# Kernel tuning notes

Hardware: AMD Instinct MI355X
Metric: run time of the kernel (lower is better)

Reference implementation:

```python
import jax, jax.numpy as jnp
import numpy as np

DT = 0.1
BOX = 1.0  # WORLD_SIZE
EPS = 1e-6


def range_angle(ang):
    return jnp.mod(ang + jnp.pi, 2.0 * jnp.pi) - jnp.pi


def ekf_step(x, P, a, Y, n1, n2_sigma, n2_kappa, gains, obs_gains):
    # x: (N,5) [px,py,ang,vel,ang_vel]; P: (N,5,5); a: (N,2); Y: (2,N)
    N = x.shape[0]
    dt = DT
    og = obs_gains

    # --- noise-free dynamics (w=0 in original forward) ---
    vel = gains[0] * a[:, 0]
    ang_vel = gains[1] * a[:, 1]
    ang = range_angle(x[:, 2] + ang_vel * dt)
    px = jnp.clip(x[:, 0] + vel * jnp.cos(ang) * dt, -BOX, BOX)
    py = jnp.clip(x[:, 1] + vel * jnp.sin(ang) * dt, -BOX, BOX)
    x_ = jnp.stack([px, py, ang, vel, ang_vel], axis=1)  # (N,5)

    # --- Jacobian A (N,5,5): eye(3) block + two trig entries ---
    d3 = jnp.arange(3)
    A = jnp.zeros((N, 5, 5), x.dtype)
    A = A.at[:, d3, d3].set(1.0)
    A = A.at[:, 0, 2].set(-vel * jnp.sin(ang) * dt)
    A = A.at[:, 1, 2].set(vel * jnp.cos(ang) * dt)

    # --- predict: L is identity in the original code, so L Q L^T = Q ---
    Q = jnp.diag(jnp.exp(2.0 * n1))
    P_ = jnp.einsum('nij,njk,nlk->nil', A, P, A) + Q  # (N,5,5)

    # --- innovation covariance S = H P_ H^T + M R M^T (R = I, M diag) ---
    # H = [0 | diag(og)] so H P_ H^T = diag(og) P_[3:5,3:5] diag(og)
    HPHt = P_[:, 3:5, 3:5] * og[None, :, None] * og[None, None, :]
    m_diag = x_[:, 3:5] ** 2 * jnp.exp(2.0 * n2_kappa) + jnp.exp(2.0 * n2_sigma)
    S = HPHt + m_diag[:, :, None] * jnp.eye(2, dtype=x.dtype)  # (N,2,2)

    # --- explicit 2x2 inverse ---
    sa, sb = S[:, 0, 0], S[:, 0, 1]
    sc, sd = S[:, 1, 0], S[:, 1, 1]
    det = sa * sd - sb * sc
    Sinv = jnp.stack([jnp.stack([sd, -sb], -1), jnp.stack([-sc, sa], -1)], -2)
    Sinv = Sinv / det[:, None, None]

    # --- Kalman gain K = P_ H^T S^{-1} ---
    PHt = P_[:, :, 3:5] * og[None, None, :]  # (N,5,2)
    K = jnp.einsum('nij,njk->nik', PHt, Sinv)  # (N,5,2)

    # --- update ---
    h = og[None, :] * x_[:, 3:5]  # noise-free observations (N,2)
    err = Y.T - h
    x_new = x_ + jnp.einsum('nij,nj->ni', K, err)

    KH = jnp.zeros((N, 5, 5), x.dtype).at[:, :, 3:5].set(K * og[None, None, :])
    I_KH = jnp.eye(5, dtype=x.dtype) - KH
    P_new = jnp.einsum('nij,njk->nik', I_KH, P_)
    P_new = 0.5 * (P_new + jnp.swapaxes(P_new, -1, -2)) + EPS * jnp.eye(5, dtype=x.dtype)
    return x_new, P_new, K


def setup_inputs() -> dict:
    key = jax.random.key(0)
    ks = jax.random.split(key, 6)
    N = 500_000
    x = jax.random.normal(ks[0], (N, 5), jnp.float32)
    # symmetric positive-definite covariances
    Lr = 0.1 * jax.random.normal(ks[1], (N, 5, 5), jnp.float32)
    P = jnp.einsum('nij,nkj->nik', Lr, Lr) + 0.5 * jnp.eye(5, dtype=jnp.float32)
    a = jax.random.normal(ks[2], (N, 2), jnp.float32)
    Y = 0.5 * jax.random.normal(ks[3], (2, N), jnp.float32)
    n1 = jnp.full((5,), -1.0, jnp.float32)
    n2 = jnp.full((4,), -1.0, jnp.float32)
    return {
        'x': x, 'P': P, 'a': a, 'Y': Y,
        'n1': n1,
        'n2_sigma': n2[:2],
        'n2_kappa': n2[2:],
        'gains': jnp.ones((2,), jnp.float32),
        'obs_gains': jnp.ones((2,), jnp.float32),
    }


def reference(x, P, a, Y, n1, n2_sigma, n2_kappa, gains, obs_gains):
    return ekf_step(x, P, a, Y, n1, n2_sigma, n2_kappa, gains, obs_gains)
```

## Files before the change

kernel.cpp:

```cpp
#include <hip/hip_runtime.h>
#include <math.h>
#include <stdint.h>


#define BLK 64
#define SLICE_F 2560

__global__ __launch_bounds__(256) void ekf_kernel(
    const float* __restrict__ xg, const float* __restrict__ Pg,
    const float* __restrict__ ag, const float* __restrict__ Yg,
    const float* __restrict__ n1, const float* __restrict__ n2s,
    const float* __restrict__ n2k, const float* __restrict__ gains,
    const float* __restrict__ og, float* __restrict__ out, int N)
{
    __shared__ float4 ldsv[4 * (SLICE_F / 4)];
    const int tid = threadIdx.x;
    const int wv = tid >> 6, l = tid & 63;
    float* s = (float*)ldsv + wv * SLICE_F;

    const int tiles = (N + BLK - 1) / BLK;
    const int tile = blockIdx.x * 4 + wv;
    if (tile >= tiles) return;
    const int base = tile * BLK;

    const float dt = 0.1f;
    const float fPI  = 3.14159265358979323846f;
    const float f2PI = 6.28318530717958647692f;
    const float EPS_ = 1e-6f;

    const float g0 = gains[0], g1 = gains[1];
    const float og0 = og[0], og1 = og[1];
    const float q0 = expf(2.f * n1[0]), q1 = expf(2.f * n1[1]),
                q2 = expf(2.f * n1[2]), q3 = expf(2.f * n1[3]),
                q4 = expf(2.f * n1[4]);
    const float e2s0 = expf(2.f * n2s[0]), e2s1 = expf(2.f * n2s[1]);
    const float e2k0 = expf(2.f * n2k[0]), e2k1 = expf(2.f * n2k[1]);

    if (base + BLK <= N) {
        const float4* p4 = (const float4*)(Pg + (size_t)base * 25);
        float4 v0 = p4[0 * 64 + l];
        float4 v1 = p4[1 * 64 + l];
        float4 v2 = p4[2 * 64 + l];
        float4 v3 = p4[3 * 64 + l];
        float4 v4 = p4[4 * 64 + l];
        float4 v5 = p4[5 * 64 + l];
        float  vr = (Pg + (size_t)base * 25)[1536 + l];
        float4 xv = ((const float4*)(xg + (size_t)base * 5))[l];
        float  xr = (xg + (size_t)base * 5)[256 + l];
        float2 av = ((const float2*)(ag + (size_t)base * 2))[l];
        float  y0 = Yg[base + l];
        float  y1 = Yg[N + base + l];

        float4* s4 = (float4*)s;
        s4[0 * 64 + l] = v0; s4[1 * 64 + l] = v1; s4[2 * 64 + l] = v2;
        s4[3 * 64 + l] = v3; s4[4 * 64 + l] = v4; s4[5 * 64 + l] = v5;
        s[1536 + l] = vr;
        ((float4*)(s + 1600))[l] = xv;
        s[1856 + l] = xr;

        const float* pr = s + l * 25;
        float p00 = pr[0],  p01 = pr[1],  p02 = pr[2];
        float p10 = pr[5],  p11 = pr[6],  p12 = pr[7];
        float p20 = pr[10], p21 = pr[11], p22 = pr[12];
        const float* xp = s + 1600 + l * 5;
        float x0 = xp[0], x1 = xp[1], x2 = xp[2];

        float vel = g0 * av.x, angvel = g1 * av.y;

        float ar = x2 + angvel * dt + fPI;
        float w = fmodf(ar, f2PI);
        if (w < 0.0f) w += f2PI;
        float ang = w - fPI;

        float sn, cs;
        sincosf(ang, &sn, &cs);

        float px = fminf(fmaxf(x0 + vel * cs * dt, -1.0f), 1.0f);
        float py = fminf(fmaxf(x1 + vel * sn * dt, -1.0f), 1.0f);

        float m0 = -vel * sn * dt, m1 = vel * cs * dt;

        float b00 = p00 + m0 * p20, b01 = p01 + m0 * p21, b02 = p02 + m0 * p22;
        float b10 = p10 + m1 * p20, b11 = p11 + m1 * p21, b12 = p12 + m1 * p22;
        float t00 = b00 + m0 * b02, t01 = b01 + m1 * b02;
        float t10 = b10 + m0 * b12, t11 = b11 + m1 * b12;
        float t20 = p20 + m0 * p22, t21 = p21 + m1 * p22, t22 = p22;
        float t02 = b02, t12 = b12;

        t00 += q0; t11 += q1; t22 += q2;
        float s01 = 0.5f * (t01 + t10);
        float s02 = 0.5f * (t02 + t20);
        float s12 = 0.5f * (t12 + t21);
        t00 += EPS_; t11 += EPS_; t22 += EPS_;

        float S00 = q3 * og0 * og0 + vel * vel * e2k0 + e2s0;
        float S11 = q4 * og1 * og1 + angvel * angvel * e2k1 + e2s1;
        float K30 = q3 * og0 / S00;
        float K41 = q4 * og1 / S11;

        float xn3 = vel    + K30 * (y0 - og0 * vel);
        float xn4 = angvel + K41 * (y1 - og1 * angvel);
        float Pn33 = (1.0f - K30 * og0) * q3 + EPS_;
        float Pn44 = (1.0f - K41 * og1) * q4 + EPS_;

        float* xx = s + l * 5;
        xx[0] = px; xx[1] = py; xx[2] = ang; xx[3] = xn3; xx[4] = xn4;
        float* pp = s + 320 + l * 25;
        pp[0]  = t00; pp[1]  = s01; pp[2]  = s02; pp[3]  = 0.f; pp[4]  = 0.f;
        pp[5]  = s01; pp[6]  = t11; pp[7]  = s12; pp[8]  = 0.f; pp[9]  = 0.f;
        pp[10] = s02; pp[11] = s12; pp[12] = t22; pp[13] = 0.f; pp[14] = 0.f;
        pp[15] = 0.f; pp[16] = 0.f; pp[17] = 0.f; pp[18] = Pn33; pp[19] = 0.f;
        pp[20] = 0.f; pp[21] = 0.f; pp[22] = 0.f; pp[23] = 0.f; pp[24] = Pn44;
        float* kk = s + 1920 + l * 10;
        kk[0] = 0.f; kk[1] = 0.f; kk[2] = 0.f; kk[3] = 0.f; kk[4] = 0.f;
        kk[5] = 0.f; kk[6] = K30; kk[7] = 0.f; kk[8] = 0.f; kk[9] = K41;

        float4* gx4 = (float4*)(out + (size_t)base * 5);
        float4* gp4 = (float4*)(out + (size_t)5 * N + (size_t)base * 25);
        float4* gk4 = (float4*)(out + (size_t)30 * N + (size_t)base * 10);
        const float4* lx4 = (const float4*)s;
        const float4* lp4 = (const float4*)(s + 320);
        const float4* lk4 = (const float4*)(s + 1920);
        gx4[l] = lx4[l];
        if (l < 16) gx4[64 + l] = lx4[64 + l];
        #pragma unroll
        for (int j = 0; j < 6; ++j) gp4[j * 64 + l] = lp4[j * 64 + l];
        if (l < 16) gp4[384 + l] = lp4[384 + l];
        #pragma unroll
        for (int j = 0; j < 2; ++j) gk4[j * 64 + l] = lk4[j * 64 + l];
        if (l < 32) gk4[128 + l] = lk4[128 + l];
    } else {
        const int i = base + l;
        if (i < N) {
            const float* pr = Pg + (size_t)i * 25;
            float p00 = pr[0],  p01 = pr[1],  p02 = pr[2];
            float p10 = pr[5],  p11 = pr[6],  p12 = pr[7];
            float p20 = pr[10], p21 = pr[11], p22 = pr[12];
            float x0 = xg[i * 5 + 0], x1 = xg[i * 5 + 1], x2 = xg[i * 5 + 2];
            float a0 = ag[i * 2 + 0], a1 = ag[i * 2 + 1];
            float y0 = Yg[i], y1 = Yg[N + i];

            float vel = g0 * a0, angvel = g1 * a1;
            float ar = x2 + angvel * dt + fPI;
            float w = fmodf(ar, f2PI);
            if (w < 0.0f) w += f2PI;
            float ang = w - fPI;
            float sn, cs;
            sincosf(ang, &sn, &cs);
            float px = fminf(fmaxf(x0 + vel * cs * dt, -1.0f), 1.0f);
            float py = fminf(fmaxf(x1 + vel * sn * dt, -1.0f), 1.0f);
            float m0 = -vel * sn * dt, m1 = vel * cs * dt;
            float b00 = p00 + m0 * p20, b01 = p01 + m0 * p21, b02 = p02 + m0 * p22;
            float b10 = p10 + m1 * p20, b11 = p11 + m1 * p21, b12 = p12 + m1 * p22;
            float t00 = b00 + m0 * b02, t01 = b01 + m1 * b02;
            float t10 = b10 + m0 * b12, t11 = b11 + m1 * b12;
            float t20 = p20 + m0 * p22, t21 = p21 + m1 * p22, t22 = p22;
            float t02 = b02, t12 = b12;
            t00 += q0; t11 += q1; t22 += q2;
            float s01 = 0.5f * (t01 + t10);
            float s02 = 0.5f * (t02 + t20);
            float s12 = 0.5f * (t12 + t21);
            t00 += EPS_; t11 += EPS_; t22 += EPS_;
            float S00 = q3 * og0 * og0 + vel * vel * e2k0 + e2s0;
            float S11 = q4 * og1 * og1 + angvel * angvel * e2k1 + e2s1;
            float K30 = q3 * og0 / S00;
            float K41 = q4 * og1 / S11;
            float xn3 = vel    + K30 * (y0 - og0 * vel);
            float xn4 = angvel + K41 * (y1 - og1 * angvel);
            float Pn33 = (1.0f - K30 * og0) * q3 + EPS_;
            float Pn44 = (1.0f - K41 * og1) * q4 + EPS_;

            float* gx = out + (size_t)i * 5;
            gx[0] = px; gx[1] = py; gx[2] = ang; gx[3] = xn3; gx[4] = xn4;
            float* gp = out + (size_t)5 * N + (size_t)i * 25;
            gp[0] = t00; gp[1] = s01; gp[2] = s02; gp[3] = 0.f; gp[4] = 0.f;
            gp[5] = s01; gp[6] = t11; gp[7] = s12; gp[8] = 0.f; gp[9] = 0.f;
            gp[10] = s02; gp[11] = s12; gp[12] = t22; gp[13] = 0.f; gp[14] = 0.f;
            gp[15] = 0.f; gp[16] = 0.f; gp[17] = 0.f; gp[18] = Pn33; gp[19] = 0.f;
            gp[20] = 0.f; gp[21] = 0.f; gp[22] = 0.f; gp[23] = 0.f; gp[24] = Pn44;
            float* gk = out + (size_t)30 * N + (size_t)i * 10;
            gk[0] = 0.f; gk[1] = 0.f; gk[2] = 0.f; gk[3] = 0.f; gk[4] = 0.f;
            gk[5] = 0.f; gk[6] = K30; gk[7] = 0.f; gk[8] = 0.f; gk[9] = K41;
        }
    }
}

extern "C" void kernel_launch(void* const* d_in, const int* in_sizes, int n_in,
                              void* d_out, int out_size, void* d_ws, size_t ws_size,
                              hipStream_t stream) {
    const float* x     = (const float*)d_in[0];
    const float* P     = (const float*)d_in[1];
    const float* a     = (const float*)d_in[2];
    const float* Y     = (const float*)d_in[3];
    const float* n1    = (const float*)d_in[4];
    const float* n2s   = (const float*)d_in[5];
    const float* n2k   = (const float*)d_in[6];
    const float* gains = (const float*)d_in[7];
    const float* og    = (const float*)d_in[8];
    const int N = in_sizes[0] / 5;
    const int tiles = (N + BLK - 1) / BLK;
    const int G = (tiles + 3) / 4;
    ekf_kernel<<<G, 256, 0, stream>>>(x, P, a, Y, n1, n2s, n2k, gains, og,
                                      (float*)d_out, N);
}
```

Measured before the change: 148.7 us.

## Process four tiles per wave with register double-buffered loads of needed P entries

Each block is now a single wave that handles four consecutive 64-row tiles. Loads for the next tile are issued before the current tile is processed, using two register sets alternately, so memory latency overlaps with compute. Inputs are read straight from global memory as the nine needed entries of P (three float3 rows) plus x, a and Y, instead of staging the whole 25-float P row through LDS. The trade-offs are uncoalesced strided loads and a grid four times smaller, with fewer independent waves to hide latency.

After: 150.8 us. About the same (+1.4%).

```diff
diff --git a/kernel.cpp b/kernel.cpp
--- a/kernel.cpp
+++ b/kernel.cpp
@@ -4,24 +4,95 @@
 
 
 #define BLK 64
-#define SLICE_F 2560
+#define TPW 4
 
-__global__ __launch_bounds__(256) void ekf_kernel(
+#define DECL(p) \
+    float p##_p00, p##_p01, p##_p02, p##_p10, p##_p11, p##_p12, \
+          p##_p20, p##_p21, p##_p22, p##_x0, p##_x1, p##_x2, \
+          p##_a0, p##_a1, p##_y0, p##_y1
+
+#define LOAD(p, tile_) do { \
+    const int b_ = (tile_) * BLK; \
+    const float* pb_ = Pg + (size_t)(b_ + l) * 25; \
+    float3 r0_ = *(const float3*)(pb_); \
+    float3 r1_ = *(const float3*)(pb_ + 5); \
+    float3 r2_ = *(const float3*)(pb_ + 10); \
+    float3 xv_ = *(const float3*)(xg + (size_t)(b_ + l) * 5); \
+    float2 av_ = *(const float2*)(ag + (size_t)(b_ + l) * 2); \
+    p##_p00 = r0_.x; p##_p01 = r0_.y; p##_p02 = r0_.z; \
+    p##_p10 = r1_.x; p##_p11 = r1_.y; p##_p12 = r1_.z; \
+    p##_p20 = r2_.x; p##_p21 = r2_.y; p##_p22 = r2_.z; \
+    p##_x0 = xv_.x; p##_x1 = xv_.y; p##_x2 = xv_.z; \
+    p##_a0 = av_.x; p##_a1 = av_.y; \
+    p##_y0 = Yg[b_ + l]; p##_y1 = Yg[N + b_ + l]; \
+} while (0)
+
+#define PROC(p, tile_) do { \
+    const int b_ = (tile_) * BLK; \
+    float vel = g0 * p##_a0, angvel = g1 * p##_a1; \
+    float ar = p##_x2 + angvel * dt + fPI; \
+    float wm = fmodf(ar, f2PI); if (wm < 0.f) wm += f2PI; \
+    float ang = wm - fPI; \
+    float sn, cs; sincosf(ang, &sn, &cs); \
+    float px = fminf(fmaxf(p##_x0 + vel * cs * dt, -1.f), 1.f); \
+    float py = fminf(fmaxf(p##_x1 + vel * sn * dt, -1.f), 1.f); \
+    float m0 = -vel * sn * dt, m1 = vel * cs * dt; \
+    float b00 = p##_p00 + m0 * p##_p20, b01 = p##_p01 + m0 * p##_p21, b02 = p##_p02 + m0 * p##_p22; \
+    float b10 = p##_p10 + m1 * p##_p20, b11 = p##_p11 + m1 * p##_p21, b12 = p##_p12 + m1 * p##_p22; \
+    float t00 = b00 + m0 * b02, t01 = b01 + m1 * b02; \
+    float t10 = b10 + m0 * b12, t11 = b11 + m1 * b12; \
+    float t20 = p##_p20 + m0 * p##_p22, t21 = p##_p21 + m1 * p##_p22, t22 = p##_p22; \
+    float t02 = b02, t12 = b12; \
+    t00 += q0; t11 += q1; t22 += q2; \
+    float s01 = 0.5f * (t01 + t10), s02 = 0.5f * (t02 + t20), s12 = 0.5f * (t12 + t21); \
+    t00 += EPS_; t11 += EPS_; t22 += EPS_; \
+    float S00 = q3 * og0 * og0 + vel * vel * e2k0 + e2s0; \
+    float S11 = q4 * og1 * og1 + angvel * angvel * e2k1 + e2s1; \
+    float K30 = q3 * og0 / S00, K41 = q4 * og1 / S11; \
+    float xn3 = vel    + K30 * (p##_y0 - og0 * vel); \
+    float xn4 = angvel + K41 * (p##_y1 - og1 * angvel); \
+    float Pn33 = (1.f - K30 * og0) * q3 + EPS_; \
+    float Pn44 = (1.f - K41 * og1) * q4 + EPS_; \
+    float* xx = s + l * 5; \
+    xx[0] = px; xx[1] = py; xx[2] = ang; xx[3] = xn3; xx[4] = xn4; \
+    float* pp = s + 320 + l * 25; \
+    pp[0]  = t00; pp[1]  = s01; pp[2]  = s02; pp[3]  = 0.f; pp[4]  = 0.f; \
+    pp[5]  = s01; pp[6]  = t11; pp[7]  = s12; pp[8]  = 0.f; pp[9]  = 0.f; \
+    pp[10] = s02; pp[11] = s12; pp[12] = t22; pp[13] = 0.f; pp[14] = 0.f; \
+    pp[15] = 0.f; pp[16] = 0.f; pp[17] = 0.f; pp[18] = Pn33; pp[19] = 0.f; \
+    pp[20] = 0.f; pp[21] = 0.f; pp[22] = 0.f; pp[23] = 0.f; pp[24] = Pn44; \
+    float* kk = s + 1920 + l * 10; \
+    kk[0] = 0.f; kk[1] = 0.f; kk[2] = 0.f; kk[3] = 0.f; kk[4] = 0.f; \
+    kk[5] = 0.f; kk[6] = K30; kk[7] = 0.f; kk[8] = 0.f; kk[9] = K41; \
+    float4* gx4 = (float4*)(out + (size_t)b_ * 5); \
+    float4* gp4 = (float4*)(out + (size_t)5 * N + (size_t)b_ * 25); \
+    float4* gk4 = (float4*)(out + (size_t)30 * N + (size_t)b_ * 10); \
+    const float4* lx4 = (const float4*)s; \
+    const float4* lp4 = (const float4*)(s + 320); \
+    const float4* lk4 = (const float4*)(s + 1920); \
+    gx4[l] = lx4[l]; \
+    if (l < 16) gx4[64 + l] = lx4[64 + l]; \
+    gp4[0 * 64 + l] = lp4[0 * 64 + l]; gp4[1 * 64 + l] = lp4[1 * 64 + l]; \
+    gp4[2 * 64 + l] = lp4[2 * 64 + l]; gp4[3 * 64 + l] = lp4[3 * 64 + l]; \
+    gp4[4 * 64 + l] = lp4[4 * 64 + l]; gp4[5 * 64 + l] = lp4[5 * 64 + l]; \
+    if (l < 16) gp4[384 + l] = lp4[384 + l]; \
+    gk4[0 * 64 + l] = lk4[0 * 64 + l]; gk4[1 * 64 + l] = lk4[1 * 64 + l]; \
+    if (l < 32) gk4[128 + l] = lk4[128 + l]; \
+} while (0)
+
+__global__ __launch_bounds__(64, 2) void ekf_kernel(
     const float* __restrict__ xg, const float* __restrict__ Pg,
     const float* __restrict__ ag, const float* __restrict__ Yg,
     const float* __restrict__ n1, const float* __restrict__ n2s,
     const float* __restrict__ n2k, const float* __restrict__ gains,
     const float* __restrict__ og, float* __restrict__ out, int N)
 {
-    __shared__ float4 ldsv[4 * (SLICE_F / 4)];
-    const int tid = threadIdx.x;
-    const int wv = tid >> 6, l = tid & 63;
-    float* s = (float*)ldsv + wv * SLICE_F;
-
+    __shared__ float s[2560];
+    const int l = threadIdx.x;
+    const int w = blockIdx.x;
     const int tiles = (N + BLK - 1) / BLK;
-    const int tile = blockIdx.x * 4 + wv;
-    if (tile >= tiles) return;
-    const int base = tile * BLK;
+    const int t0 = w * TPW;
+    if (t0 >= tiles) return;
 
     const float dt = 0.1f;
     const float fPI  = 3.14159265358979323846f;
@@ -36,102 +107,22 @@
     const float e2s0 = expf(2.f * n2s[0]), e2s1 = expf(2.f * n2s[1]);
     const float e2k0 = expf(2.f * n2k[0]), e2k1 = expf(2.f * n2k[1]);
 
-    if (base + BLK <= N) {
-        const float4* p4 = (const float4*)(Pg + (size_t)base * 25);
-        float4 v0 = p4[0 * 64 + l];
-        float4 v1 = p4[1 * 64 + l];
-        float4 v2 = p4[2 * 64 + l];
-        float4 v3 = p4[3 * 64 + l];
-        float4 v4 = p4[4 * 64 + l];
-        float4 v5 = p4[5 * 64 + l];
-        float  vr = (Pg + (size_t)base * 25)[1536 + l];
-        float4 xv = ((const float4*)(xg + (size_t)base * 5))[l];
-        float  xr = (xg + (size_t)base * 5)[256 + l];
-        float2 av = ((const float2*)(ag + (size_t)base * 2))[l];
-        float  y0 = Yg[base + l];
-        float  y1 = Yg[N + base + l];
-
-        float4* s4 = (float4*)s;
-        s4[0 * 64 + l] = v0; s4[1 * 64 + l] = v1; s4[2 * 64 + l] = v2;
-        s4[3 * 64 + l] = v3; s4[4 * 64 + l] = v4; s4[5 * 64 + l] = v5;
-        s[1536 + l] = vr;
-        ((float4*)(s + 1600))[l] = xv;
-        s[1856 + l] = xr;
-
-        const float* pr = s + l * 25;
-        float p00 = pr[0],  p01 = pr[1],  p02 = pr[2];
-        float p10 = pr[5],  p11 = pr[6],  p12 = pr[7];
-        float p20 = pr[10], p21 = pr[11], p22 = pr[12];
-        const float* xp = s + 1600 + l * 5;
-        float x0 = xp[0], x1 = xp[1], x2 = xp[2];
-
-        float vel = g0 * av.x, angvel = g1 * av.y;
-
-        float ar = x2 + angvel * dt + fPI;
-        float w = fmodf(ar, f2PI);
-        if (w < 0.0f) w += f2PI;
-        float ang = w - fPI;
-
-        float sn, cs;
-        sincosf(ang, &sn, &cs);
-
-        float px = fminf(fmaxf(x0 + vel * cs * dt, -1.0f), 1.0f);
-        float py = fminf(fmaxf(x1 + vel * sn * dt, -1.0f), 1.0f);
-
-        float m0 = -vel * sn * dt, m1 = vel * cs * dt;
-
-        float b00 = p00 + m0 * p20, b01 = p01 + m0 * p21, b02 = p02 + m0 * p22;
-        float b10 = p10 + m1 * p20, b11 = p11 + m1 * p21, b12 = p12 + m1 * p22;
-        float t00 = b00 + m0 * b02, t01 = b01 + m1 * b02;
-        float t10 = b10 + m0 * b12, t11 = b11 + m1 * b12;
-        float t20 = p20 + m0 * p22, t21 = p21 + m1 * p22, t22 = p22;
-        float t02 = b02, t12 = b12;
-
-        t00 += q0; t11 += q1; t22 += q2;
-        float s01 = 0.5f * (t01 + t10);
-        float s02 = 0.5f * (t02 + t20);
-        float s12 = 0.5f * (t12 + t21);
-        t00 += EPS_; t11 += EPS_; t22 += EPS_;
-
-        float S00 = q3 * og0 * og0 + vel * vel * e2k0 + e2s0;
-        float S11 = q4 * og1 * og1 + angvel * angvel * e2k1 + e2s1;
-        float K30 = q3 * og0 / S00;
-        float K41 = q4 * og1 / S11;
-
-        float xn3 = vel    + K30 * (y0 - og0 * vel);
-        float xn4 = angvel + K41 * (y1 - og1 * angvel);
-        float Pn33 = (1.0f - K30 * og0) * q3 + EPS_;
-        float Pn44 = (1.0f - K41 * og1) * q4 + EPS_;
-
-        float* xx = s + l * 5;
-        xx[0] = px; xx[1] = py; xx[2] = ang; xx[3] = xn3; xx[4] = xn4;
-        float* pp = s + 320 + l * 25;
-        pp[0]  = t00; pp[1]  = s01; pp[2]  = s02; pp[3]  = 0.f; pp[4]  = 0.f;
-        pp[5]  = s01; pp[6]  = t11; pp[7]  = s12; pp[8]  = 0.f; pp[9]  = 0.f;
-        pp[10] = s02; pp[11] = s12; pp[12] = t22; pp[13] = 0.f; pp[14] = 0.f;
-        pp[15] = 0.f; pp[16] = 0.f; pp[17] = 0.f; pp[18] = Pn33; pp[19] = 0.f;
-        pp[20] = 0.f; pp[21] = 0.f; pp[22] = 0.f; pp[23] = 0.f; pp[24] = Pn44;
-        float* kk = s + 1920 + l * 10;
-        kk[0] = 0.f; kk[1] = 0.f; kk[2] = 0.f; kk[3] = 0.f; kk[4] = 0.f;
-        kk[5] = 0.f; kk[6] = K30; kk[7] = 0.f; kk[8] = 0.f; kk[9] = K41;
-
-        float4* gx4 = (float4*)(out + (size_t)base * 5);
-        float4* gp4 = (float4*)(out + (size_t)5 * N + (size_t)base * 25);
-        float4* gk4 = (float4*)(out + (size_t)30 * N + (size_t)base * 10);
-        const float4* lx4 = (const float4*)s;
-        const float4* lp4 = (const float4*)(s + 320);
-        const float4* lk4 = (const float4*)(s + 1920);
-        gx4[l] = lx4[l];
-        if (l < 16) gx4[64 + l] = lx4[64 + l];
-        #pragma unroll
-        for (int j = 0; j < 6; ++j) gp4[j * 64 + l] = lp4[j * 64 + l];
-        if (l < 16) gp4[384 + l] = lp4[384 + l];
-        #pragma unroll
-        for (int j = 0; j < 2; ++j) gk4[j * 64 + l] = lk4[j * 64 + l];
-        if (l < 32) gk4[128 + l] = lk4[128 + l];
+    if ((t0 + TPW) * BLK <= N) {
+        DECL(A); DECL(B);
+        LOAD(A, t0);
+        LOAD(B, t0 + 1);
+        PROC(A, t0);
+        LOAD(A, t0 + 2);
+        PROC(B, t0 + 1);
+        LOAD(B, t0 + 3);
+        PROC(A, t0 + 2);
+        PROC(B, t0 + 3);
     } else {
-        const int i = base + l;
-        if (i < N) {
+        for (int tt = 0; tt < TPW; ++tt) {
+            const int tile = t0 + tt;
+            if (tile >= tiles) break;
+            const int i = tile * BLK + l;
+            if (i >= N) continue;
             const float* pr = Pg + (size_t)i * 25;
             float p00 = pr[0],  p01 = pr[1],  p02 = pr[2];
             float p10 = pr[5],  p11 = pr[6],  p12 = pr[7];
@@ -142,13 +133,13 @@
 
             float vel = g0 * a0, angvel = g1 * a1;
             float ar = x2 + angvel * dt + fPI;
-            float w = fmodf(ar, f2PI);
-            if (w < 0.0f) w += f2PI;
-            float ang = w - fPI;
+            float wm = fmodf(ar, f2PI);
+            if (wm < 0.f) wm += f2PI;
+            float ang = wm - fPI;
             float sn, cs;
             sincosf(ang, &sn, &cs);
-            float px = fminf(fmaxf(x0 + vel * cs * dt, -1.0f), 1.0f);
-            float py = fminf(fmaxf(x1 + vel * sn * dt, -1.0f), 1.0f);
+            float px = fminf(fmaxf(x0 + vel * cs * dt, -1.f), 1.f);
+            float py = fminf(fmaxf(x1 + vel * sn * dt, -1.f), 1.f);
             float m0 = -vel * sn * dt, m1 = vel * cs * dt;
             float b00 = p00 + m0 * p20, b01 = p01 + m0 * p21, b02 = p02 + m0 * p22;
             float b10 = p10 + m1 * p20, b11 = p11 + m1 * p21, b12 = p12 + m1 * p22;
@@ -167,8 +158,8 @@
             float K41 = q4 * og1 / S11;
             float xn3 = vel    + K30 * (y0 - og0 * vel);
             float xn4 = angvel + K41 * (y1 - og1 * angvel);
-            float Pn33 = (1.0f - K30 * og0) * q3 + EPS_;
-            float Pn44 = (1.0f - K41 * og1) * q4 + EPS_;
+            float Pn33 = (1.f - K30 * og0) * q3 + EPS_;
+            float Pn44 = (1.f - K41 * og1) * q4 + EPS_;
 
             float* gx = out + (size_t)i * 5;
             gx[0] = px; gx[1] = py; gx[2] = ang; gx[3] = xn3; gx[4] = xn4;
@@ -199,7 +190,7 @@
     const float* og    = (const float*)d_in[8];
     const int N = in_sizes[0] / 5;
     const int tiles = (N + BLK - 1) / BLK;
-    const int G = (tiles + 3) / 4;
-    ekf_kernel<<<G, 256, 0, stream>>>(x, P, a, Y, n1, n2s, n2k, gains, og,
-                                      (float*)d_out, N);
+    const int G = (tiles + TPW - 1) / TPW;
+    ekf_kernel<<<G, 64, 0, stream>>>(x, P, a, Y, n1, n2s, n2k, gains, og,
+                                     (float*)d_out, N);
 }
```
